# Optimization experiments

Measured on AMD Instinct MI355X. Metric: run time of the kernel, lower is better.

Reference implementation:

```python
import jax, jax.numpy as jnp
import numpy as np

DECAY = 0.2
THRESH = 0.8


def setup_inputs() -> dict:
    key = jax.random.key(0)
    ks = jax.random.split(key, 5)
    B, T, Cin, H, W = 16, 15, 64, 56, 56
    Cout = 128
    x = jax.random.normal(ks[0], (B, T, Cin, H, W), dtype=jnp.float32)
    # torch conv init then *5; random normal scaled similarly
    fan_in = Cin * 3 * 3
    conv_w = jax.random.normal(ks[1], (Cout, Cin, 3, 3), dtype=jnp.float32) * (5.0 / np.sqrt(fan_in))
    conv_b = jax.random.normal(ks[2], (Cout,), dtype=jnp.float32) * (1.0 / np.sqrt(fan_in))
    fc_w = jax.random.normal(ks[3], (1, 3), dtype=jnp.float32) * (1.0 / np.sqrt(3.0))
    fc_b = jax.random.normal(ks[4], (1,), dtype=jnp.float32) * (1.0 / np.sqrt(3.0))
    return {"x": x, "conv_w": conv_w, "conv_b": conv_b, "fc_w": fc_w, "fc_b": fc_b, "wins": 15}


def _act_fun(v):
    # step function (surrogate gradient only matters in bwd module)
    return (v > 0.0).astype(v.dtype)


def _conv(x_t, conv_w, conv_b):
    out = jax.lax.conv_general_dilated(
        x_t, conv_w, window_strides=(1, 1), padding=((1, 1), (1, 1)),
        dimension_numbers=("NCHW", "OIHW", "NCHW"))
    return out + conv_b[None, :, None, None]


def _fc(m3, fc_w, fc_b):
    # Linear(3,1) over last axis: [B,C,H,W,3] -> [B,C,H,W]
    return jnp.einsum("bchwi,i->bchw", m3, fc_w[0]) + fc_b[0]


def _avg_pool2(s):
    B, C, H, W = s.shape
    return s.reshape(B, C, H // 2, 2, W // 2, 2).mean(axis=(3, 5))


def reference(x, conv_w, conv_b, fc_w, fc_b, wins):
    B, T, Cin, H, W = x.shape
    Cout = conv_w.shape[0]
    mem0 = jnp.zeros((B, Cout, H, W, 4), dtype=x.dtype)
    spike0 = jnp.zeros((B, Cout, H, W), dtype=x.dtype)

    def step(carry, x_t):
        mem, spike = carry
        conv_out = _conv(x_t, conv_w, conv_b)  # [B,Cout,H,W]
        # inner input computed from OLD mem channels 0:3 (matches update_neuron)
        x4 = _fc(mem[..., 0:3], fc_w, fc_b)
        decayed = mem * (DECAY * (1.0 - spike))[..., None]
        new03 = decayed[..., 0:3] + conv_out[..., None]
        new3 = decayed[..., 3] + x4
        mem_new = jnp.concatenate([new03, new3[..., None]], axis=-1)
        mem1 = _fc(mem_new[..., 0:3], fc_w, fc_b) + mem_new[..., 3]
        spike_new = _act_fun(mem1 - THRESH)
        return (mem_new, spike_new), _avg_pool2(spike_new)

    xs = jnp.transpose(x[:, :wins], (1, 0, 2, 3, 4))  # [T,B,Cin,H,W]
    _, spikes = jax.lax.scan(step, (mem0, spike0), xs)
    return jnp.transpose(spikes, (1, 0, 2, 3, 4))  # [B,T,Cout,H/2,W/2]
```

## Files before the change

kernel.cpp:

```cpp
#include <hip/hip_runtime.h>

#define B_N 16
#define T_N 15
#define CIN 64
#define COUT 128
#define HS 56
#define HWN 3136
#define NSG (16 * 128 * 28 * 28)


__global__ void wt_kernel(const float* __restrict__ w, float* __restrict__ wt4) {
    int i = blockIdx.x * 256 + threadIdx.x;
    if (i >= COUT * 576) return;
    int co = i / 576;
    int r = i - co * 576;
    int ci = r / 9;
    int kk = r - ci * 9;
    wt4[((size_t)kk * CIN + ci) * COUT + co] = w[i];
}

__global__ __launch_bounds__(256) void conv_direct(
    const float* __restrict__ x, const float* __restrict__ wt4,
    const float* __restrict__ bias, float* __restrict__ obuf,
    int t0, int nz)
{
    const int bid = blockIdx.x;
    const int z = (bid & 7) * (nz >> 3) + (bid >> 3);

    const int tile = z % 49;
    const int u = z / 49;
    const int b = u & 15;
    const int tc = u >> 4;

    const int ty = tile / 7, tx = tile - ty * 7;
    const int h0 = ty * 8, w0c = tx * 8;

    const int tid = threadIdx.x;
    const int lane = tid & 63;
    const int wv = __builtin_amdgcn_readfirstlane(tid >> 6);
    const int co0 = wv * 32;
    const int lh = lane >> 3;
    const int lw = lane & 7;
    const int h = h0 + lh;
    const int wq = w0c + lw;

    const float* xb = x + ((size_t)(b * T_N + (t0 + tc)) * CIN) * HWN;

    float acc[32];
#pragma unroll
    for (int j = 0; j < 32; ++j) acc[j] = 0.0f;

    for (int kh = 0; kh < 3; ++kh) {
        const int gh = h - 1 + kh;
        for (int kw = 0; kw < 3; ++kw) {
            const int gw = wq - 1 + kw;
            const bool ok = ((unsigned)gh < (unsigned)HS) &&
                            ((unsigned)gw < (unsigned)HS);
            const int off = ok ? gh * HS + gw : 0;
            const float* wk = wt4 + ((size_t)(kh * 3 + kw) * CIN) * COUT + co0;
#pragma unroll 4
            for (int ci = 0; ci < CIN; ++ci) {
                float xv = xb[(size_t)ci * HWN + off];
                xv = ok ? xv : 0.0f;
#pragma unroll
                for (int j = 0; j < 32; ++j) {
                    acc[j] = fmaf(xv, wk[ci * COUT + j], acc[j]);
                }
            }
        }
    }

    const size_t obase = ((size_t)(tc * 16 + b) * COUT + co0) * HWN
                       + (size_t)h * HS + wq;
#pragma unroll
    for (int j = 0; j < 32; ++j) {
        obuf[obase + (size_t)j * HWN] = __fadd_rn(acc[j], bias[co0 + j]);
    }
}

__global__ __launch_bounds__(256) void rec32(
    const float* __restrict__ cvbuf, const float* __restrict__ fcw,
    const float* __restrict__ fcb, float* __restrict__ stateD,
    unsigned* __restrict__ stateS, float* __restrict__ out,
    int t0, int nt, int doLoad, int doStore)
{
    const int idx = blockIdx.x * 256 + threadIdx.x;
    const int pw = idx % 28;
    int tmp = idx / 28;
    const int ph = tmp % 28;
    tmp /= 28;
    const int co = tmp & 127;
    const int b = tmp >> 7;

    const size_t g = (size_t)idx;

    const float w0 = fcw[0], w1 = fcw[1], w2 = fcw[2], fb = fcb[0];

    float u[4], m3[4], s[4];
    if (doLoad) {
        unsigned sm = stateS[g];
#pragma unroll
        for (int p = 0; p < 4; ++p) {
            u[p] = stateD[(size_t)p * NSG + g];
            m3[p] = stateD[(size_t)(4 + p) * NSG + g];
            s[p] = (float)((sm >> p) & 1u);
        }
    } else {
#pragma unroll
        for (int p = 0; p < 4; ++p) { u[p] = 0.0f; m3[p] = 0.0f; s[p] = 0.0f; }
    }

    const int h0 = ph * 2, wc0 = pw * 2;

    for (int tc = 0; tc < nt; ++tc) {
        const size_t cbase = ((size_t)(tc * 16 + b) * COUT + co) * HWN
                           + (size_t)h0 * HS + wc0;
        const float cv[4] = {cvbuf[cbase], cvbuf[cbase + 1],
                             cvbuf[cbase + HS], cvbuf[cbase + HS + 1]};

#pragma unroll
        for (int p = 0; p < 4; ++p) {
            float e0 = __fadd_rn(__fadd_rn(__fmul_rn(u[p], w0), __fmul_rn(u[p], w1)),
                                 __fmul_rn(u[p], w2));
            float x4 = __fadd_rn(e0, fb);
            float dd = __fmul_rn(0.2f, __fsub_rn(1.0f, s[p]));
            u[p]  = __fadd_rn(__fmul_rn(u[p], dd), cv[p]);
            m3[p] = __fadd_rn(__fmul_rn(m3[p], dd), x4);
            float e1 = __fadd_rn(__fadd_rn(__fmul_rn(u[p], w0), __fmul_rn(u[p], w1)),
                                 __fmul_rn(u[p], w2));
            float mem1 = __fadd_rn(__fadd_rn(e1, fb), m3[p]);
            s[p] = (__fsub_rn(mem1, 0.8f) > 0.0f) ? 1.0f : 0.0f;
        }

        float pooled = 0.25f * (((s[0] + s[1]) + s[2]) + s[3]);
        out[(((size_t)b * T_N + (t0 + tc)) * COUT + co) * 784 + ph * 28 + pw] = pooled;
    }

    if (doStore) {
        unsigned sm = 0;
#pragma unroll
        for (int p = 0; p < 4; ++p) {
            stateD[(size_t)p * NSG + g] = u[p];
            stateD[(size_t)(4 + p) * NSG + g] = m3[p];
            sm |= (s[p] > 0.5f) ? (1u << p) : 0u;
        }
        stateS[g] = sm;
    }
}

extern "C" void kernel_launch(void* const* d_in, const int* in_sizes, int n_in,
                              void* d_out, int out_size, void* d_ws, size_t ws_size,
                              hipStream_t stream) {
    const float* x     = (const float*)d_in[0];
    const float* cw    = (const float*)d_in[1];
    const float* cbias = (const float*)d_in[2];
    const float* fcw   = (const float*)d_in[3];
    const float* fcb   = (const float*)d_in[4];
    float* out = (float*)d_out;

    const size_t wtB   = (size_t)576 * COUT * sizeof(float);
    const size_t convT = (size_t)B_N * COUT * HWN * sizeof(float);
    const size_t statB = (size_t)NSG * 8 * sizeof(float)
                       + (size_t)NSG * sizeof(unsigned);

    int Tc;
    if (wtB + (size_t)T_N * convT <= ws_size) {
        Tc = T_N;
    } else if (ws_size > wtB + statB + convT) {
        Tc = (int)((ws_size - wtB - statB) / convT);
        if (Tc > T_N) Tc = T_N;
    } else {
        return;
    }

    float* wt4 = (float*)d_ws;
    float* convbuf = (float*)((char*)d_ws + wtB);
    float* stateD = (float*)((char*)d_ws + wtB + (size_t)Tc * convT);
    unsigned* stateS = (unsigned*)((char*)stateD + (size_t)NSG * 8 * sizeof(float));

    wt_kernel<<<(COUT * 576 + 255) / 256, 256, 0, stream>>>(cw, wt4);

    for (int t0 = 0; t0 < T_N; t0 += Tc) {
        const int nt = (T_N - t0 < Tc) ? (T_N - t0) : Tc;
        const int nz = nt * 16 * 49;
        conv_direct<<<nz, 256, 0, stream>>>(x, wt4, cbias, convbuf, t0, nz);
        rec32<<<NSG / 256, 256, 0, stream>>>(
            convbuf, fcw, fcb, stateD, stateS, out,
            t0, nt, t0 > 0 ? 1 : 0, (t0 + nt) < T_N ? 1 : 0);
    }
}
```

Before: 1.620 ms.

## Transpose input to padded NHWC and remap conv to channel-per-lane tiles

Input frames are first zeroed and transposed into a padded channels-last buffer, so the convolution reads float4 channel vectors without any bounds checks. Each lane now owns one output channel and accumulates a 4x8 pixel tile, loading weights per lane while the input vectors are shared across the wave. Outputs are staged through shared memory so stores to the NCHW buffer are coalesced. This adds a zeroing pass, a transpose pass and a larger workspace in exchange for better conv load efficiency.

```diff
diff --git a/kernel.cpp b/kernel.cpp
--- a/kernel.cpp
+++ b/kernel.cpp
@@ -6,6 +6,7 @@
 #define COUT 128
 #define HS 56
 #define HWN 3136
+#define XSP 3364
 #define NSG (16 * 128 * 28 * 28)
 
 
@@ -19,62 +20,113 @@
     wt4[((size_t)kk * CIN + ci) * COUT + co] = w[i];
 }
 
-__global__ __launch_bounds__(256) void conv_direct(
-    const float* __restrict__ x, const float* __restrict__ wt4,
-    const float* __restrict__ bias, float* __restrict__ obuf,
-    int t0, int nz)
+__global__ void zero_xs(float4* __restrict__ p, long n4) {
+    long i = (long)blockIdx.x * 256 + threadIdx.x;
+    long stride = (long)gridDim.x * 256;
+    for (; i < n4; i += stride) p[i] = make_float4(0.f, 0.f, 0.f, 0.f);
+}
+
+__global__ __launch_bounds__(256) void tr_kernel(
+    const float* __restrict__ x, float* __restrict__ xs, int t0)
 {
+    __shared__ float t[64][65];
+    const int blk = blockIdx.x;
+    const int hwt = blk % 49;
+    const int btc = blk / 49;
+    const int b = btc & 15;
+    const int tt = t0 + (btc >> 4);
+    const int hw0 = hwt * 64;
+    const int tid = threadIdx.x;
+
+    const float* xb = x + ((size_t)(b * T_N + tt) * CIN) * HWN;
+#pragma unroll
+    for (int k = 0; k < 16; ++k) {
+        int ci = (tid >> 6) * 16 + k;
+        int hwl = tid & 63;
+        t[ci][hwl] = xb[(size_t)ci * HWN + hw0 + hwl];
+    }
+    __syncthreads();
+#pragma unroll
+    for (int k = 0; k < 16; ++k) {
+        int hwl = (tid >> 6) * 16 + k;
+        int ci = tid & 63;
+        int hw = hw0 + hwl;
+        int ph = hw / 56, pw = hw - ph * 56;
+        xs[((size_t)btc * XSP + (ph + 1) * 58 + (pw + 1)) * CIN + ci] = t[ci][hwl];
+    }
+}
+
+__global__ __launch_bounds__(256) void conv_smem(
+    const float* __restrict__ xs, const float* __restrict__ wt4,
+    const float* __restrict__ bias, float* __restrict__ obuf, int nz)
+{
+    __shared__ float tb[4][16 * 68];
+
     const int bid = blockIdx.x;
-    const int z = (bid & 7) * (nz >> 3) + (bid >> 3);
-
-    const int tile = z % 49;
-    const int u = z / 49;
-    const int b = u & 15;
-    const int tc = u >> 4;
-
-    const int ty = tile / 7, tx = tile - ty * 7;
-    const int h0 = ty * 8, w0c = tx * 8;
-
-    const int tid = threadIdx.x;
-    const int lane = tid & 63;
-    const int wv = __builtin_amdgcn_readfirstlane(tid >> 6);
-    const int co0 = wv * 32;
-    const int lh = lane >> 3;
-    const int lw = lane & 7;
-    const int h = h0 + lh;
-    const int wq = w0c + lw;
-
-    const float* xb = x + ((size_t)(b * T_N + (t0 + tc)) * CIN) * HWN;
+    const int zb = (bid & 7) * (nz >> 3) + (bid >> 3);
+
+    const int lane = threadIdx.x & 63;
+    const int wslot = threadIdx.x >> 6;
+    const int wid = __builtin_amdgcn_readfirstlane(zb * 4 + wslot);
+
+    const int ch = wid & 1;
+    const int rh = (wid >> 1) & 1;
+    const int rest = wid >> 2;
+    const int tile = rest % 49;
+    const int btc = rest / 49;
+
+    const int h0 = (tile / 7) * 8 + rh * 4;
+    const int w0c = (tile % 7) * 8;
+    const int co = ch * 64 + lane;
+
+    const float* xsb = xs + (size_t)btc * XSP * CIN;
 
     float acc[32];
 #pragma unroll
-    for (int j = 0; j < 32; ++j) acc[j] = 0.0f;
+    for (int i = 0; i < 32; ++i) acc[i] = 0.0f;
 
     for (int kh = 0; kh < 3; ++kh) {
-        const int gh = h - 1 + kh;
         for (int kw = 0; kw < 3; ++kw) {
-            const int gw = wq - 1 + kw;
-            const bool ok = ((unsigned)gh < (unsigned)HS) &&
-                            ((unsigned)gw < (unsigned)HS);
-            const int off = ok ? gh * HS + gw : 0;
-            const float* wk = wt4 + ((size_t)(kh * 3 + kw) * CIN) * COUT + co0;
-#pragma unroll 4
-            for (int ci = 0; ci < CIN; ++ci) {
-                float xv = xb[(size_t)ci * HWN + off];
-                xv = ok ? xv : 0.0f;
-#pragma unroll
-                for (int j = 0; j < 32; ++j) {
-                    acc[j] = fmaf(xv, wk[ci * COUT + j], acc[j]);
+            const float* xtap = xsb + ((size_t)((h0 + kh) * 58 + (w0c + kw))) * CIN;
+            const float* wtap = wt4 + ((size_t)(kh * 3 + kw) * CIN) * COUT + co;
+            for (int c8 = 0; c8 < 16; ++c8) {
+                const float wv0 = wtap[(c8 * 4 + 0) * COUT];
+                const float wv1 = wtap[(c8 * 4 + 1) * COUT];
+                const float wv2 = wtap[(c8 * 4 + 2) * COUT];
+                const float wv3 = wtap[(c8 * 4 + 3) * COUT];
+                const float* xc = xtap + c8 * 4;
+#pragma unroll
+                for (int i = 0; i < 32; ++i) {
+                    const float4 xq = *(const float4*)(xc + ((i >> 3) * 58 + (i & 7)) * CIN);
+                    acc[i] = fmaf(xq.x, wv0, acc[i]);
+                    acc[i] = fmaf(xq.y, wv1, acc[i]);
+                    acc[i] = fmaf(xq.z, wv2, acc[i]);
+                    acc[i] = fmaf(xq.w, wv3, acc[i]);
                 }
             }
         }
     }
 
-    const size_t obase = ((size_t)(tc * 16 + b) * COUT + co0) * HWN
-                       + (size_t)h * HS + wq;
-#pragma unroll
-    for (int j = 0; j < 32; ++j) {
-        obuf[obase + (size_t)j * HWN] = __fadd_rn(acc[j], bias[co0 + j]);
+    const float bv = bias[co];
+#pragma unroll
+    for (int i = 0; i < 32; ++i) acc[i] = __fadd_rn(acc[i], bv);
+
+    float* T = &tb[wslot][0];
+    const size_t obase = (size_t)(btc * COUT) * HWN;
+#pragma unroll
+    for (int c = 0; c < 2; ++c) {
+#pragma unroll
+        for (int i = 0; i < 16; ++i) T[i * 68 + lane] = acc[c * 16 + i];
+#pragma unroll
+        for (int r = 0; r < 16; ++r) {
+            const int col = (lane >> 4) + r * 4;
+            const int pxl = (lane & 15);
+            const float v = T[pxl * 68 + col];
+            const int px = c * 16 + pxl;
+            const int hh = h0 + (px >> 3);
+            const int ww = w0c + (px & 7);
+            obuf[obase + (size_t)(ch * 64 + col) * HWN + hh * HS + ww] = v;
+        }
     }
 }
 
@@ -160,14 +212,15 @@
 
     const size_t wtB   = (size_t)576 * COUT * sizeof(float);
     const size_t convT = (size_t)B_N * COUT * HWN * sizeof(float);
+    const size_t xsT   = (size_t)B_N * XSP * CIN * sizeof(float);
     const size_t statB = (size_t)NSG * 8 * sizeof(float)
                        + (size_t)NSG * sizeof(unsigned);
 
     int Tc;
-    if (wtB + (size_t)T_N * convT <= ws_size) {
+    if (wtB + (size_t)T_N * (convT + xsT) <= ws_size) {
         Tc = T_N;
-    } else if (ws_size > wtB + statB + convT) {
-        Tc = (int)((ws_size - wtB - statB) / convT);
+    } else if (ws_size > wtB + statB + convT + xsT) {
+        Tc = (int)((ws_size - wtB - statB) / (convT + xsT));
         if (Tc > T_N) Tc = T_N;
     } else {
         return;
@@ -175,15 +228,20 @@
 
     float* wt4 = (float*)d_ws;
     float* convbuf = (float*)((char*)d_ws + wtB);
-    float* stateD = (float*)((char*)d_ws + wtB + (size_t)Tc * convT);
+    float* xsbuf = (float*)((char*)d_ws + wtB + (size_t)Tc * convT);
+    float* stateD = (float*)((char*)d_ws + wtB + (size_t)Tc * (convT + xsT));
     unsigned* stateS = (unsigned*)((char*)stateD + (size_t)NSG * 8 * sizeof(float));
 
     wt_kernel<<<(COUT * 576 + 255) / 256, 256, 0, stream>>>(cw, wt4);
 
     for (int t0 = 0; t0 < T_N; t0 += Tc) {
         const int nt = (T_N - t0 < Tc) ? (T_N - t0) : Tc;
-        const int nz = nt * 16 * 49;
-        conv_direct<<<nz, 256, 0, stream>>>(x, wt4, cbias, convbuf, t0, nz);
+        const int nbt = nt * 16;
+        const long n4 = (long)nbt * XSP * CIN / 4;
+        zero_xs<<<2048, 256, 0, stream>>>((float4*)xsbuf, n4);
+        tr_kernel<<<nbt * 49, 256, 0, stream>>>(x, xsbuf, t0);
+        const int nz = nbt * 49;
+        conv_smem<<<nz, 256, 0, stream>>>(xsbuf, wt4, cbias, convbuf, nz);
         rec32<<<NSG / 256, 256, 0, stream>>>(
             convbuf, fcw, fcb, stateD, stateS, out,
             t0, nt, t0 > 0 ? 1 : 0, (t0 + nt) < T_N ? 1 : 0);
```

After: 3.226 ms. 1.99x slower.
